# Kernel optimization log

Hardware: AMD Instinct MI355X
Metric: run time of the kernel (lower is better)

## Reference

```python
import jax, jax.numpy as jnp
import numpy as np

N = 50000   # nodes
E = 800000  # edges (avg degree 16)
D0 = 256    # input feat dim
H1, D1 = 4, 64  # layer1 heads, per-head dim
H2, D2 = 4, 64  # layer2 heads, per-head dim
NEG_SLOPE = 0.2


def setup_inputs() -> dict:
    key = jax.random.key(0)
    ks = jax.random.split(key, 9)
    s = 0.1
    feature = jax.random.normal(ks[0], (N, D0), jnp.float32)
    src = jax.random.randint(ks[1], (E,), 0, N, dtype=jnp.int32)
    dst = jax.random.randint(ks[2], (E,), 0, N, dtype=jnp.int32)
    W1 = jax.random.normal(ks[3], (D0, H1 * D1), jnp.float32) * s
    al1 = jax.random.normal(ks[4], (H1, D1), jnp.float32) * s
    ar1 = jax.random.normal(ks[5], (H1, D1), jnp.float32) * s
    W2 = jax.random.normal(ks[6], (H1 * D1, H2 * D2), jnp.float32) * s
    al2 = jax.random.normal(ks[7], (H2, D2), jnp.float32) * s
    ar2 = jax.random.normal(ks[8], (H2, D2), jnp.float32) * s
    return dict(feature=feature, W1=W1, al1=al1, ar1=ar1,
                W2=W2, al2=al2, ar2=ar2, src=src, dst=dst)


def gat_conv(x, W, al, ar, src, dst, H, d, act):
    # x: [N, in]; W: [in, H*d]; al, ar: [H, d]
    feat = (x @ W).reshape(N, H, d)                 # [N,H,d]
    el = jnp.einsum('nhd,hd->nh', feat, al)         # [N,H] src-side score
    er = jnp.einsum('nhd,hd->nh', feat, ar)         # [N,H] dst-side score
    e = jax.nn.leaky_relu(el[src] + er[dst], NEG_SLOPE)  # [E,H]
    # segment softmax over edges grouped by destination node
    m = jax.ops.segment_max(e, dst, num_segments=N)      # [N,H]
    ex = jnp.exp(e - m[dst])                             # [E,H]
    denom = jax.ops.segment_sum(ex, dst, num_segments=N) # [N,H]
    alpha = ex / jnp.maximum(denom[dst], 1e-9)           # [E,H]
    msg = feat[src] * alpha[..., None]                   # [E,H,d]
    out = jax.ops.segment_sum(msg, dst, num_segments=N)  # [N,H,d]
    return act(out)


def reference(feature, W1, al1, ar1, W2, al2, ar2, src, dst):
    h = gat_conv(feature, W1, al1, ar1, src, dst, H1, D1, jax.nn.elu)  # [N,H1,D1]
    h = h.reshape(N, H1 * D1)                                          # concat heads
    h = gat_conv(h, W2, al2, ar2, src, dst, H2, D2, lambda x: x)       # [N,H2,D2]
    return h.mean(axis=1)                                              # mean over heads -> [N,D2]
```

## Files before the change

### kernel.cpp

```cpp
#include <hip/hip_runtime.h>
#include <hip/hip_fp16.h>
#include <math.h>
#include <stdint.h>

#define NNODES 50000
#define NEDGES 800000
#define DIM 256
#define HEADS 4
#define DH 64
#define NEG_SLOPE 0.2f

#define CSR_NPB 1024
#define CSR_NB ((NNODES + CSR_NPB - 1) / CSR_NPB)

typedef _Float16 half8 __attribute__((ext_vector_type(8)));
typedef float floatx4 __attribute__((ext_vector_type(4)));

static __device__ __forceinline__ float h2f(unsigned short h) {
  __half x = *(const __half*)&h;
  return __half2float(x);
}
static __device__ __forceinline__ unsigned short f2h(float f) {
  __half x = __float2half(f);
  return *(const unsigned short*)&x;
}

__global__ __launch_bounds__(256) void wt_k(const float* __restrict__ W1,
                                            const float* __restrict__ W2,
                                            _Float16* __restrict__ WT1,
                                            _Float16* __restrict__ WT2) {
  int b = blockIdx.x;
  const float* W = (b < 256) ? W1 : W2;
  _Float16* WT = (b < 256) ? WT1 : WT2;
  int n = b & 255;
  int k = threadIdx.x;
  WT[n * 256 + k] = (_Float16)W[k * 256 + n];
}

template <typename AT>
__global__ __launch_bounds__(256) void gemm_k(const AT* __restrict__ A,
                                              const _Float16* __restrict__ BT,
                                              const float* __restrict__ alw,
                                              const float* __restrict__ arw,
                                              unsigned short* __restrict__ Cb,
                                              float* __restrict__ el,
                                              float* __restrict__ er, int M) {
  int t = threadIdx.x;
  int lane = t & 63, w = t >> 6;
  int m16 = lane & 15, q = lane >> 4;
  int row0 = blockIdx.x * 64;
  floatx4 acc[4][4];
#pragma unroll
  for (int i = 0; i < 4; ++i)
#pragma unroll
    for (int j = 0; j < 4; ++j) acc[i][j] = (floatx4){0.f, 0.f, 0.f, 0.f};

  float4 alv[4], arv[4];
#pragma unroll
  for (int ni = 0; ni < 4; ++ni) {
    alv[ni] = *(const float4*)&alw[w * 64 + ni * 16 + q * 4];
    arv[ni] = *(const float4*)&arw[w * 64 + ni * 16 + q * 4];
  }

  const AT* ab[4];
  const _Float16* bb[4];
#pragma unroll
  for (int i = 0; i < 4; ++i) {
    int ar = row0 + i * 16 + m16;
    if (ar > M - 1) ar = M - 1;
    ab[i] = &A[(size_t)ar * DIM + q * 8];
    bb[i] = &BT[(size_t)(w * 64 + i * 16 + m16) * DIM + q * 8];
  }

#pragma unroll
  for (int k0 = 0; k0 < DIM; k0 += 32) {
    half8 wf[4], af[4];
#pragma unroll
    for (int i = 0; i < 4; ++i) wf[i] = *(const half8*)(bb[i] + k0);
#pragma unroll
    for (int i = 0; i < 4; ++i) {
      if constexpr (sizeof(AT) == 4) {
        float4 x0 = *(const float4*)(ab[i] + k0);
        float4 x1 = *(const float4*)(ab[i] + k0 + 4);
        half8 hv;
        hv[0] = (_Float16)x0.x; hv[1] = (_Float16)x0.y;
        hv[2] = (_Float16)x0.z; hv[3] = (_Float16)x0.w;
        hv[4] = (_Float16)x1.x; hv[5] = (_Float16)x1.y;
        hv[6] = (_Float16)x1.z; hv[7] = (_Float16)x1.w;
        af[i] = hv;
      } else {
        af[i] = *(const half8*)(ab[i] + k0);
      }
    }
#pragma unroll
    for (int mi = 0; mi < 4; ++mi)
#pragma unroll
      for (int ni = 0; ni < 4; ++ni)
        acc[mi][ni] = __builtin_amdgcn_mfma_f32_16x16x32_f16(
            wf[ni], af[mi], acc[mi][ni], 0, 0, 0);
  }

#pragma unroll
  for (int mi = 0; mi < 4; ++mi) {
    int node = row0 + mi * 16 + m16;
    float pl = 0.f, pr = 0.f;
#pragma unroll
    for (int ni = 0; ni < 4; ++ni) {
      pl += acc[mi][ni][0] * alv[ni].x + acc[mi][ni][1] * alv[ni].y +
            acc[mi][ni][2] * alv[ni].z + acc[mi][ni][3] * alv[ni].w;
      pr += acc[mi][ni][0] * arv[ni].x + acc[mi][ni][1] * arv[ni].y +
            acc[mi][ni][2] * arv[ni].z + acc[mi][ni][3] * arv[ni].w;
    }
    pl += __shfl_xor(pl, 16, 64); pl += __shfl_xor(pl, 32, 64);
    pr += __shfl_xor(pr, 16, 64); pr += __shfl_xor(pr, 32, 64);
    if (q == 0 && node < M) {
      el[node * HEADS + w] = pl;
      er[node * HEADS + w] = pr;
    }
    if (node < M) {
#pragma unroll
      for (int ni = 0; ni < 4; ++ni) {
        ushort4 o;
        o.x = f2h(acc[mi][ni][0]); o.y = f2h(acc[mi][ni][1]);
        o.z = f2h(acc[mi][ni][2]); o.w = f2h(acc[mi][ni][3]);
        *(ushort4*)&Cb[(size_t)node * DIM + w * 64 + ni * 16 + q * 4] = o;
      }
    }
  }
}

__global__ __launch_bounds__(256) void deg_k(const int* __restrict__ dst,
                                             int* __restrict__ deg) {
  int e4 = (blockIdx.x * 256 + threadIdx.x) * 4;
  if (e4 < NEDGES) {
    int4 d = *(const int4*)&dst[e4];
    atomicAdd(&deg[d.x], 1);
    atomicAdd(&deg[d.y], 1);
    atomicAdd(&deg[d.z], 1);
    atomicAdd(&deg[d.w], 1);
  }
}

__global__ __launch_bounds__(256) void csr_part_k(const int* __restrict__ deg,
                                                  int* __restrict__ bsum) {
  __shared__ int ws[4];
  int t = threadIdx.x, lane = t & 63, w = t >> 6;
  int idx = blockIdx.x * CSR_NPB + t * 4;
  int s = 0;
  if (idx < NNODES) {
    int4 v = *(const int4*)&deg[idx];
    s = v.x + v.y + v.z + v.w;
  }
#pragma unroll
  for (int off = 1; off < 64; off <<= 1) s += __shfl_xor(s, off, 64);
  if (lane == 0) ws[w] = s;
  __syncthreads();
  if (t == 0) bsum[blockIdx.x] = ws[0] + ws[1] + ws[2] + ws[3];
}

__global__ __launch_bounds__(64) void csr_mid_k(const int* __restrict__ bsum,
                                                int* __restrict__ bbase,
                                                int* __restrict__ row_ptr) {
  int t = threadIdx.x;
  int v = (t < CSR_NB) ? bsum[t] : 0;
  int incl = v;
#pragma unroll
  for (int off = 1; off < 64; off <<= 1) {
    int u = __shfl_up(incl, off, 64);
    if (t >= off) incl += u;
  }
  if (t < CSR_NB) bbase[t] = incl - v;
  if (t == 0) row_ptr[NNODES] = NEDGES;
}

__global__ __launch_bounds__(256) void csr_emit_k(const int* __restrict__ deg,
                                                  const int* __restrict__ bbase,
                                                  int* __restrict__ row_ptr,
                                                  int* __restrict__ cursor) {
  __shared__ int ws[4];
  int t = threadIdx.x, lane = t & 63, w = t >> 6;
  int idx = blockIdx.x * CSR_NPB + t * 4;
  int4 v = make_int4(0, 0, 0, 0);
  if (idx < NNODES) v = *(const int4*)&deg[idx];
  int s0 = v.x, s1 = s0 + v.y, s2 = s1 + v.z, s3 = s2 + v.w;
  int incl = s3;
#pragma unroll
  for (int off = 1; off < 64; off <<= 1) {
    int u = __shfl_up(incl, off, 64);
    if (lane >= off) incl += u;
  }
  if (lane == 63) ws[w] = incl;
  __syncthreads();
  int wbase = 0;
#pragma unroll
  for (int i = 0; i < 4; ++i)
    if (i < w) wbase += ws[i];
  int base = bbase[blockIdx.x] + wbase + incl - s3;
  if (idx < NNODES) {
    int4 rp = make_int4(base, base + s0, base + s1, base + s2);
    *(int4*)&row_ptr[idx] = rp;
    *(int4*)&cursor[idx] = rp;
  }
}

__global__ __launch_bounds__(256) void scatter_k(const int* __restrict__ src,
                                                 const int* __restrict__ dst,
                                                 int* __restrict__ cursor,
                                                 int* __restrict__ srcoff) {
  int e4 = (blockIdx.x * 256 + threadIdx.x) * 4;
  if (e4 < NEDGES) {
    int4 s = *(const int4*)&src[e4];
    int4 d = *(const int4*)&dst[e4];
    int p;
    p = atomicAdd(&cursor[d.x], 1); srcoff[p] = s.x << 9;
    p = atomicAdd(&cursor[d.y], 1); srcoff[p] = s.y << 9;
    p = atomicAdd(&cursor[d.z], 1); srcoff[p] = s.z << 9;
    p = atomicAdd(&cursor[d.w], 1); srcoff[p] = s.w << 9;
  }
}

template <int MODE>
__global__ __launch_bounds__(256) void agg_k(const unsigned short* __restrict__ feat,
                                             const float* __restrict__ el,
                                             const float* __restrict__ er,
                                             const int* __restrict__ row_ptr,
                                             const int* __restrict__ srcoff,
                                             void* __restrict__ outp) {
  int lane = threadIdx.x & 63;
  int w = threadIdx.x >> 6;
  int n = blockIdx.x * 4 + w;
  if (n >= NNODES) return;
  int h = lane >> 4;
  int hsel = lane & 3;
  int esel = lane >> 2;
  int beg = row_ptr[n], end = row_ptr[n + 1];
  float erv = er[n * HEADS + hsel];
  int laneByte = lane * 8;
  const char* fb = (const char*)feat;
  const char* elb = (const char*)el;
  float a0 = 0.f, a1 = 0.f, a2 = 0.f, a3 = 0.f, sume = 0.f;
  for (int c0 = beg; c0 < end; c0 += 16) {
    int soff = 0;
    if (lane < 16 && c0 + lane < end) soff = srcoff[c0 + lane];
    float av = 0.f;
    if (c0 + esel < end) {
      int sE = __shfl(soff, esel, 64);
      float elv = *(const float*)(elb + (sE >> 5) + hsel * 4);
      float v = elv + erv;
      v = v > 0.f ? v : NEG_SLOPE * v;
      av = __expf(v);
    }
#pragma unroll
    for (int j = 0; j < 16; ++j) {
      int sB = __shfl(soff, j, 64);
      float a = __shfl(av, 4 * j + h, 64);
      ushort4 u = *(const ushort4*)(fb + (sB + laneByte));
      a0 += h2f(u.x) * a;
      a1 += h2f(u.y) * a;
      a2 += h2f(u.z) * a;
      a3 += h2f(u.w) * a;
      sume += a;
    }
  }
  float inv = 1.f / fmaxf(sume, 1e-9f);
  a0 *= inv; a1 *= inv; a2 *= inv; a3 *= inv;
  if (MODE == 1) {
    a0 = a0 > 0.f ? a0 : (__expf(a0) - 1.f);
    a1 = a1 > 0.f ? a1 : (__expf(a1) - 1.f);
    a2 = a2 > 0.f ? a2 : (__expf(a2) - 1.f);
    a3 = a3 > 0.f ? a3 : (__expf(a3) - 1.f);
    ushort4 o;
    o.x = f2h(a0); o.y = f2h(a1); o.z = f2h(a2); o.w = f2h(a3);
    *(ushort4*)((char*)outp + (size_t)n * 512 + laneByte) = o;
  } else {
    a0 += __shfl_xor(a0, 16, 64); a0 += __shfl_xor(a0, 32, 64);
    a1 += __shfl_xor(a1, 16, 64); a1 += __shfl_xor(a1, 32, 64);
    a2 += __shfl_xor(a2, 16, 64); a2 += __shfl_xor(a2, 32, 64);
    a3 += __shfl_xor(a3, 16, 64); a3 += __shfl_xor(a3, 32, 64);
    if (lane < 16) {
      float4 o = make_float4(a0 * 0.25f, a1 * 0.25f, a2 * 0.25f, a3 * 0.25f);
      *(float4*)((float*)outp + (size_t)n * 64 + lane * 4) = o;
    }
  }
}

extern "C" void kernel_launch(void* const* d_in, const int* in_sizes, int n_in,
                              void* d_out, int out_size, void* d_ws, size_t ws_size,
                              hipStream_t stream) {
  const float* feature = (const float*)d_in[0];
  const float* W1 = (const float*)d_in[1];
  const float* al1 = (const float*)d_in[2];
  const float* ar1 = (const float*)d_in[3];
  const float* W2 = (const float*)d_in[4];
  const float* al2 = (const float*)d_in[5];
  const float* ar2 = (const float*)d_in[6];
  const int* src = (const int*)d_in[7];
  const int* dst = (const int*)d_in[8];
  float* out = (float*)d_out;

  uintptr_t p = (uintptr_t)d_ws;
  auto alloc = [&](size_t bytes) -> void* {
    uintptr_t cur = (p + 255) & ~(uintptr_t)255;
    p = cur + bytes;
    return (void*)cur;
  };
  unsigned short* featH = (unsigned short*)alloc((size_t)NNODES * DIM * 2);
  unsigned short* hidH  = (unsigned short*)alloc((size_t)NNODES * DIM * 2);
  _Float16* WT1 = (_Float16*)alloc((size_t)256 * 256 * 2);
  _Float16* WT2 = (_Float16*)alloc((size_t)256 * 256 * 2);
  float* el    = (float*)alloc((size_t)NNODES * HEADS * 4);
  float* er    = (float*)alloc((size_t)NNODES * HEADS * 4);
  int* deg     = (int*)alloc((size_t)NNODES * 4);
  int* row_ptr = (int*)alloc((size_t)(NNODES + 1) * 4);
  int* cursor  = (int*)alloc((size_t)NNODES * 4);
  int* srcoff  = (int*)alloc((size_t)NEDGES * 4);
  int* bsum    = (int*)alloc((size_t)CSR_NB * 4);
  int* bbase   = (int*)alloc((size_t)CSR_NB * 4);

  const int E4B = (NEDGES / 4 + 255) / 256;
  const int MB = (NNODES + 63) / 64;
  const int AB = (NNODES + 3) / 4;

  wt_k<<<512, 256, 0, stream>>>(W1, W2, WT1, WT2);
  hipMemsetAsync(deg, 0, (size_t)NNODES * 4, stream);
  deg_k<<<E4B, 256, 0, stream>>>(dst, deg);
  csr_part_k<<<CSR_NB, 256, 0, stream>>>(deg, bsum);
  csr_mid_k<<<1, 64, 0, stream>>>(bsum, bbase, row_ptr);
  csr_emit_k<<<CSR_NB, 256, 0, stream>>>(deg, bbase, row_ptr, cursor);
  scatter_k<<<E4B, 256, 0, stream>>>(src, dst, cursor, srcoff);

  gemm_k<float><<<MB, 256, 0, stream>>>(feature, WT1, al1, ar1, featH, el, er, NNODES);
  agg_k<1><<<AB, 256, 0, stream>>>(featH, el, er, row_ptr, srcoff, hidH);

  gemm_k<_Float16><<<MB, 256, 0, stream>>>((const _Float16*)hidH, WT2, al2, ar2,
                                           featH, el, er, NNODES);
  agg_k<2><<<AB, 256, 0, stream>>>(featH, el, er, row_ptr, srcoff, out);
}
```

Before: 401.0 us.

## Stage GEMM tiles through LDS and batch eight edges per thread in CSR build

```diff
diff --git a/kernel.cpp b/kernel.cpp
--- a/kernel.cpp
+++ b/kernel.cpp
@@ -45,6 +45,8 @@
                                               unsigned short* __restrict__ Cb,
                                               float* __restrict__ el,
                                               float* __restrict__ er, int M) {
+  __shared__ __attribute__((aligned(16))) _Float16 Asl[64][72];
+  __shared__ __attribute__((aligned(16))) _Float16 Bsl[256][72];
   int t = threadIdx.x;
   int lane = t & 63, w = t >> 6;
   int m16 = lane & 15, q = lane >> 4;
@@ -62,42 +64,63 @@
     arv[ni] = *(const float4*)&arw[w * 64 + ni * 16 + q * 4];
   }
 
-  const AT* ab[4];
-  const _Float16* bb[4];
-#pragma unroll
-  for (int i = 0; i < 4; ++i) {
-    int ar = row0 + i * 16 + m16;
-    if (ar > M - 1) ar = M - 1;
-    ab[i] = &A[(size_t)ar * DIM + q * 8];
-    bb[i] = &BT[(size_t)(w * 64 + i * 16 + m16) * DIM + q * 8];
-  }
-
-#pragma unroll
-  for (int k0 = 0; k0 < DIM; k0 += 32) {
-    half8 wf[4], af[4];
-#pragma unroll
-    for (int i = 0; i < 4; ++i) wf[i] = *(const half8*)(bb[i] + k0);
-#pragma unroll
-    for (int i = 0; i < 4; ++i) {
-      if constexpr (sizeof(AT) == 4) {
-        float4 x0 = *(const float4*)(ab[i] + k0);
-        float4 x1 = *(const float4*)(ab[i] + k0 + 4);
-        half8 hv;
-        hv[0] = (_Float16)x0.x; hv[1] = (_Float16)x0.y;
-        hv[2] = (_Float16)x0.z; hv[3] = (_Float16)x0.w;
-        hv[4] = (_Float16)x1.x; hv[5] = (_Float16)x1.y;
-        hv[6] = (_Float16)x1.z; hv[7] = (_Float16)x1.w;
-        af[i] = hv;
-      } else {
-        af[i] = *(const half8*)(ab[i] + k0);
+  int arow = t >> 2, akoff = (t & 3) * 16;
+
+  for (int k0 = 0; k0 < DIM; k0 += 64) {
+    if constexpr (sizeof(AT) == 4) {
+      float4 x0 = make_float4(0.f, 0.f, 0.f, 0.f), x1 = x0, x2 = x0, x3 = x0;
+      if (row0 + arow < M) {
+        const float* ap = (const float*)&A[(size_t)(row0 + arow) * DIM + k0 + akoff];
+        x0 = *(const float4*)ap;
+        x1 = *(const float4*)(ap + 4);
+        x2 = *(const float4*)(ap + 8);
+        x3 = *(const float4*)(ap + 12);
       }
-    }
-#pragma unroll
-    for (int mi = 0; mi < 4; ++mi)
-#pragma unroll
-      for (int ni = 0; ni < 4; ++ni)
-        acc[mi][ni] = __builtin_amdgcn_mfma_f32_16x16x32_f16(
-            wf[ni], af[mi], acc[mi][ni], 0, 0, 0);
+      half8 h0, h1;
+      h0[0] = (_Float16)x0.x; h0[1] = (_Float16)x0.y;
+      h0[2] = (_Float16)x0.z; h0[3] = (_Float16)x0.w;
+      h0[4] = (_Float16)x1.x; h0[5] = (_Float16)x1.y;
+      h0[6] = (_Float16)x1.z; h0[7] = (_Float16)x1.w;
+      h1[0] = (_Float16)x2.x; h1[1] = (_Float16)x2.y;
+      h1[2] = (_Float16)x2.z; h1[3] = (_Float16)x2.w;
+      h1[4] = (_Float16)x3.x; h1[5] = (_Float16)x3.y;
+      h1[6] = (_Float16)x3.z; h1[7] = (_Float16)x3.w;
+      *(half8*)&Asl[arow][akoff] = h0;
+      *(half8*)&Asl[arow][akoff + 8] = h1;
+    } else {
+      int4 x0 = make_int4(0, 0, 0, 0), x1 = x0;
+      if (row0 + arow < M) {
+        const AT* ap = &A[(size_t)(row0 + arow) * DIM + k0 + akoff];
+        x0 = *(const int4*)ap;
+        x1 = *(const int4*)(ap + 8);
+      }
+      *(int4*)&Asl[arow][akoff] = x0;
+      *(int4*)&Asl[arow][akoff + 8] = x1;
+    }
+    {
+      const _Float16* bp = &BT[(size_t)t * 256 + k0];
+#pragma unroll
+      for (int c = 0; c < 8; ++c)
+        *(int4*)&Bsl[t][c * 8] = *(const int4*)(bp + c * 8);
+    }
+    __syncthreads();
+    half8 wf[2][4], af[2][4];
+#pragma unroll
+    for (int s = 0; s < 2; ++s)
+#pragma unroll
+      for (int i = 0; i < 4; ++i) {
+        wf[s][i] = *(const half8*)&Bsl[w * 64 + i * 16 + m16][s * 32 + q * 8];
+        af[s][i] = *(const half8*)&Asl[i * 16 + m16][s * 32 + q * 8];
+      }
+#pragma unroll
+    for (int s = 0; s < 2; ++s)
+#pragma unroll
+      for (int mi = 0; mi < 4; ++mi)
+#pragma unroll
+        for (int ni = 0; ni < 4; ++ni)
+          acc[mi][ni] = __builtin_amdgcn_mfma_f32_16x16x32_f16(
+              wf[s][ni], af[s][mi], acc[mi][ni], 0, 0, 0);
+    __syncthreads();
   }
 
 #pragma unroll
@@ -131,13 +154,18 @@
 
 __global__ __launch_bounds__(256) void deg_k(const int* __restrict__ dst,
                                              int* __restrict__ deg) {
-  int e4 = (blockIdx.x * 256 + threadIdx.x) * 4;
-  if (e4 < NEDGES) {
-    int4 d = *(const int4*)&dst[e4];
-    atomicAdd(&deg[d.x], 1);
-    atomicAdd(&deg[d.y], 1);
-    atomicAdd(&deg[d.z], 1);
-    atomicAdd(&deg[d.w], 1);
+  int e8 = (blockIdx.x * 256 + threadIdx.x) * 8;
+  if (e8 < NEDGES) {
+    int4 d0 = *(const int4*)&dst[e8];
+    int4 d1 = *(const int4*)&dst[e8 + 4];
+    atomicAdd(&deg[d0.x], 1);
+    atomicAdd(&deg[d0.y], 1);
+    atomicAdd(&deg[d0.z], 1);
+    atomicAdd(&deg[d0.w], 1);
+    atomicAdd(&deg[d1.x], 1);
+    atomicAdd(&deg[d1.y], 1);
+    atomicAdd(&deg[d1.z], 1);
+    atomicAdd(&deg[d1.w], 1);
   }
 }
 
@@ -207,15 +235,28 @@
                                                  const int* __restrict__ dst,
                                                  int* __restrict__ cursor,
                                                  int* __restrict__ srcoff) {
-  int e4 = (blockIdx.x * 256 + threadIdx.x) * 4;
-  if (e4 < NEDGES) {
-    int4 s = *(const int4*)&src[e4];
-    int4 d = *(const int4*)&dst[e4];
-    int p;
-    p = atomicAdd(&cursor[d.x], 1); srcoff[p] = s.x << 9;
-    p = atomicAdd(&cursor[d.y], 1); srcoff[p] = s.y << 9;
-    p = atomicAdd(&cursor[d.z], 1); srcoff[p] = s.z << 9;
-    p = atomicAdd(&cursor[d.w], 1); srcoff[p] = s.w << 9;
+  int e8 = (blockIdx.x * 256 + threadIdx.x) * 8;
+  if (e8 < NEDGES) {
+    int4 s0 = *(const int4*)&src[e8];
+    int4 s1 = *(const int4*)&src[e8 + 4];
+    int4 d0 = *(const int4*)&dst[e8];
+    int4 d1 = *(const int4*)&dst[e8 + 4];
+    int p0 = atomicAdd(&cursor[d0.x], 1);
+    int p1 = atomicAdd(&cursor[d0.y], 1);
+    int p2 = atomicAdd(&cursor[d0.z], 1);
+    int p3 = atomicAdd(&cursor[d0.w], 1);
+    int p4 = atomicAdd(&cursor[d1.x], 1);
+    int p5 = atomicAdd(&cursor[d1.y], 1);
+    int p6 = atomicAdd(&cursor[d1.z], 1);
+    int p7 = atomicAdd(&cursor[d1.w], 1);
+    srcoff[p0] = s0.x << 9;
+    srcoff[p1] = s0.y << 9;
+    srcoff[p2] = s0.z << 9;
+    srcoff[p3] = s0.w << 9;
+    srcoff[p4] = s1.x << 9;
+    srcoff[p5] = s1.y << 9;
+    srcoff[p6] = s1.z << 9;
+    srcoff[p7] = s1.w << 9;
   }
 }
 
@@ -317,17 +358,17 @@
   int* bsum    = (int*)alloc((size_t)CSR_NB * 4);
   int* bbase   = (int*)alloc((size_t)CSR_NB * 4);
 
-  const int E4B = (NEDGES / 4 + 255) / 256;
+  const int E8B = (NEDGES / 8 + 255) / 256;
   const int MB = (NNODES + 63) / 64;
   const int AB = (NNODES + 3) / 4;
 
   wt_k<<<512, 256, 0, stream>>>(W1, W2, WT1, WT2);
   hipMemsetAsync(deg, 0, (size_t)NNODES * 4, stream);
-  deg_k<<<E4B, 256, 0, stream>>>(dst, deg);
+  deg_k<<<E8B, 256, 0, stream>>>(dst, deg);
   csr_part_k<<<CSR_NB, 256, 0, stream>>>(deg, bsum);
   csr_mid_k<<<1, 64, 0, stream>>>(bsum, bbase, row_ptr);
   csr_emit_k<<<CSR_NB, 256, 0, stream>>>(deg, bbase, row_ptr, cursor);
-  scatter_k<<<E4B, 256, 0, stream>>>(src, dst, cursor, srcoff);
+  scatter_k<<<E8B, 256, 0, stream>>>(src, dst, cursor, srcoff);
 
   gemm_k<float><<<MB, 256, 0, stream>>>(feature, WT1, al1, ar1, featH, el, er, NNODES);
   agg_k<1><<<AB, 256, 0, stream>>>(featH, el, er, row_ptr, srcoff, hidH);
```

Result: faster. 356.5 us (-11.1%).
